# Optimization experiments

Hardware: AMD Instinct MI355X
Metric: run time of the kernel (lower is better)

## Reference

```python
import jax, jax.numpy as jnp
import numpy as np

NUM_EXPERTS = 3
INPUT_DIM = 1024
HIDDEN_DIM = 4096
OUTPUT_DIM = 1024
ROUTER_HIDDEN = 128
BATCH = 8192


def setup_inputs() -> dict:
    key = jax.random.key(0)
    ks = jax.random.split(key, 6)
    s_in = 1.0 / np.sqrt(INPUT_DIM)
    s_h = 1.0 / np.sqrt(HIDDEN_DIM)
    s_rh = 1.0 / np.sqrt(ROUTER_HIDDEN)
    return {
        "x": jax.random.normal(ks[0], (BATCH, INPUT_DIM), jnp.float32),
        "router_w1": jax.random.normal(ks[1], (INPUT_DIM, ROUTER_HIDDEN), jnp.float32) * s_in,
        "router_b1": jnp.zeros((ROUTER_HIDDEN,), jnp.float32),
        "router_w2": jax.random.normal(ks[2], (ROUTER_HIDDEN, NUM_EXPERTS), jnp.float32) * s_rh,
        "router_b2": jnp.zeros((NUM_EXPERTS,), jnp.float32),
        "expert_w1": jax.random.normal(ks[3], (NUM_EXPERTS, INPUT_DIM, HIDDEN_DIM), jnp.float32) * s_in,
        "expert_b1": jnp.zeros((NUM_EXPERTS, HIDDEN_DIM), jnp.float32),
        "expert_w2": jax.random.normal(ks[4], (NUM_EXPERTS, HIDDEN_DIM, OUTPUT_DIM), jnp.float32) * s_h,
        "expert_b2": jnp.zeros((NUM_EXPERTS, OUTPUT_DIM), jnp.float32),
    }


def reference(x, router_w1, router_b1, router_w2, router_b2,
              expert_w1, expert_b1, expert_w2, expert_b2):
    # Router: MLP -> softmax probs, hard top-1 selection (argmax)
    rh = jax.nn.relu(x @ router_w1 + router_b1)          # [B, 128]
    logits = rh @ router_w2 + router_b2                   # [B, E]
    probs = jax.nn.softmax(logits, axis=-1)
    selected = jnp.argmax(probs, axis=-1)                 # [B] int

    # Per-expert forward on all tokens (dense equivalent of masked dispatch)
    h = jax.nn.relu(jnp.einsum('bi,eih->ebh', x, expert_w1) + expert_b1[:, None, :])  # [E,B,H]
    y = jnp.einsum('ebh,eho->ebo', h, expert_w2) + expert_b2[:, None, :]              # [E,B,O]

    # Scatter-combine: each token takes its selected expert's output
    outputs = jnp.take_along_axis(
        y, selected[None, :, None], axis=0)[0]            # [B, O]

    # routing_stats: tokens per expert
    routing_stats = jnp.bincount(selected, length=NUM_EXPERTS)
    return outputs, routing_stats
```

## Files before the change

### kernel.cpp

```cpp
#include <hip/hip_runtime.h>
#include <hip/hip_bf16.h>

typedef short bf16x8 __attribute__((ext_vector_type(8)));
typedef float f32x4 __attribute__((ext_vector_type(4)));
typedef __attribute__((address_space(1))) const void gconst_t;
typedef __attribute__((address_space(3))) void lds_t;

#define DEVI __device__ __forceinline__

constexpr int BATCH   = 8192;
constexpr int IN_DIM  = 1024;
constexpr int HID     = 4096;
constexpr int OUT_DIM = 1024;
constexpr int NE      = 3;

constexpr size_t XBF_OFF  = 0;
constexpr size_t W1T_OFF  = 16777216;
constexpr size_t W2T_OFF  = W1T_OFF + 25165824;
constexpr size_t H_OFF    = W2T_OFF + 25165824;
constexpr size_t META_OFF = H_OFF + 67108864;

DEVI unsigned short f2bf(float f) {
  __hip_bfloat16 h = __float2bfloat16(f);
  return *reinterpret_cast<unsigned short*>(&h);
}

__global__ __launch_bounds__(256) void prep_kernel(
    const float* __restrict__ x, const float* __restrict__ ew1, const float* __restrict__ ew2,
    const float* __restrict__ rw1, const float* __restrict__ rb1,
    const float* __restrict__ rw2, const float* __restrict__ rb2,
    unsigned short* __restrict__ xb, unsigned short* __restrict__ w1t,
    unsigned short* __restrict__ w2t, int* __restrict__ counts, int* __restrict__ toklist) {
  __shared__ float smem[8 * 1024 + 8 * 128];
  const int b = blockIdx.x;
  const int tid = threadIdx.x;

  if (b < 1024) {
    const int t0 = b * 8;
    float* xs = smem;
    float* rh = smem + 8 * 1024;
    {
      const float4* src = (const float4*)(x + (size_t)t0 * 1024);
      float4* dstv = (float4*)xs;
      for (int i = tid; i < 2048; i += 256) dstv[i] = src[i];
    }
    __syncthreads();
    const int g = tid >> 7, hcol = tid & 127;
    float acc[4] = {0.f, 0.f, 0.f, 0.f};
    for (int k = 0; k < 1024; k += 4) {
      const float w0 = rw1[(k + 0) * 128 + hcol];
      const float w1v = rw1[(k + 1) * 128 + hcol];
      const float w2v = rw1[(k + 2) * 128 + hcol];
      const float w3v = rw1[(k + 3) * 128 + hcol];
#pragma unroll
      for (int tt = 0; tt < 4; tt++) {
        const float4 xv = *(const float4*)&xs[(g * 4 + tt) * 1024 + k];
        acc[tt] = fmaf(xv.x, w0, acc[tt]);
        acc[tt] = fmaf(xv.y, w1v, acc[tt]);
        acc[tt] = fmaf(xv.z, w2v, acc[tt]);
        acc[tt] = fmaf(xv.w, w3v, acc[tt]);
      }
    }
    const float bb1 = rb1[hcol];
#pragma unroll
    for (int tt = 0; tt < 4; tt++)
      rh[(g * 4 + tt) * 128 + hcol] = fmaxf(acc[tt] + bb1, 0.f);
    __syncthreads();
    float* lg = smem;
    if (tid < 24) {
      const int t = tid / 3, e = tid % 3;
      float s = rb2[e];
      for (int j = 0; j < 128; j++) s = fmaf(rh[t * 128 + j], rw2[j * 3 + e], s);
      lg[t * 3 + e] = s;
    }
    __syncthreads();
    if (tid < 8) {
      const float l0 = lg[tid * 3], l1 = lg[tid * 3 + 1], l2 = lg[tid * 3 + 2];
      int sel = 0; float m = l0;
      if (l1 > m) { m = l1; sel = 1; }
      if (l2 > m) { m = l2; sel = 2; }
      const int slot = atomicAdd(&counts[sel], 1);
      toklist[sel * BATCH + slot] = t0 + tid;
    }
  } else if (b < 7168) {
    float (*tile)[65] = (float(*)[65])smem;
    const float* src; unsigned short* dst; int R, C, r0, c0;
    if (b < 4096) {
      const int bb = b - 1024, e = bb / 1024, w = bb % 1024;
      src = ew1 + (size_t)e * 1024 * 4096; dst = w1t + (size_t)e * 4096 * 1024;
      R = 1024; C = 4096; r0 = (w & 15) * 64; c0 = (w >> 4) * 64;
    } else {
      const int bb = b - 4096, e = bb / 1024, w = bb % 1024;
      src = ew2 + (size_t)e * 4096 * 1024; dst = w2t + (size_t)e * 1024 * 4096;
      R = 4096; C = 1024; r0 = (w & 63) * 64; c0 = (w >> 6) * 64;
    }
    const int tr = tid >> 4;
    const int tc = (tid & 15) << 2;
#pragma unroll
    for (int i = 0; i < 4; i++) {
      const int r = tr + i * 16;
      const float4 v = *(const float4*)(src + (size_t)(r0 + r) * C + (c0 + tc));
      tile[r][tc + 0] = v.x; tile[r][tc + 1] = v.y; tile[r][tc + 2] = v.z; tile[r][tc + 3] = v.w;
    }
    __syncthreads();
#pragma unroll
    for (int i = 0; i < 4; i++) {
      const int c = tr + i * 16;
      ushort4 o;
      o.x = f2bf(tile[tc + 0][c]);
      o.y = f2bf(tile[tc + 1][c]);
      o.z = f2bf(tile[tc + 2][c]);
      o.w = f2bf(tile[tc + 3][c]);
      *(ushort4*)(dst + (size_t)(c0 + c) * R + (r0 + tc)) = o;
    }
  } else {
    const float4* xv4 = (const float4*)x;
    const int total = BATCH * IN_DIM / 4;
    for (int i = (b - 7168) * 256 + tid; i < total; i += 512 * 256) {
      const float4 v = xv4[i];
      ushort4 o;
      o.x = f2bf(v.x); o.y = f2bf(v.y); o.z = f2bf(v.z); o.w = f2bf(v.w);
      ((ushort4*)xb)[i] = o;
    }
  }
}

template <int MODE>
__global__ __launch_bounds__(256, 2) void moe_gemm(
    const unsigned short* __restrict__ Abase, const unsigned short* __restrict__ Ball,
    const float* __restrict__ biasAll, unsigned short* __restrict__ Hout,
    float* __restrict__ Yout, const int* __restrict__ toklist, const int* __restrict__ counts,
    float* __restrict__ tail) {
  constexpr int N = (MODE == 0) ? HID : OUT_DIM;
  constexpr int K = (MODE == 0) ? IN_DIM : HID;
  constexpr int NT = K / 64;

  if (MODE == 0 && blockIdx.x == 0 && blockIdx.y == 0 && threadIdx.x < NE)
    tail[threadIdx.x] = (float)counts[threadIdx.x];

  const int c0 = counts[0], c1 = counts[1], c2 = counts[2];
  const int mb0 = (c0 + 127) >> 7, mb1 = (c1 + 127) >> 7, mb2 = (c2 + 127) >> 7;
  const int bx = blockIdx.x;
  int e, mblk;
  if (bx < mb0) { e = 0; mblk = bx; }
  else if (bx < mb0 + mb1) { e = 1; mblk = bx - mb0; }
  else if (bx < mb0 + mb1 + mb2) { e = 2; mblk = bx - mb0 - mb1; }
  else return;
  const int cnt = (e == 0) ? c0 : (e == 1) ? c1 : c2;
  const int m0 = mblk * 128;
  const int n0 = blockIdx.y * 128;
  const int off_e = (e > 0 ? c0 : 0) + (e > 1 ? c1 : 0);
  const unsigned short* Bmat = Ball + (size_t)e * ((size_t)N * K);
  const float* bias = biasAll + (size_t)e * N;

  __shared__ unsigned short Ab[2][128 * 64];
  __shared__ unsigned short Bb[2][128 * 64];

  const int tid = threadIdx.x;
  const unsigned short* aptr[4];
  const unsigned short* bptr[4];
  unsigned ldsoff[4];
#pragma unroll
  for (int l = 0; l < 4; l++) {
    const unsigned o = l * 4096u + (unsigned)tid * 16u;
    const unsigned p = o ^ (((o >> 7) & 7u) << 4);
    const int row = (int)(p >> 7);
    const int kel = (int)((p & 127u) >> 1);
    ldsoff[l] = o;
    bptr[l] = Bmat + (size_t)(n0 + row) * K + kel;
    int slot = m0 + row; if (slot > cnt - 1) slot = cnt - 1;
    const size_t arow = (MODE == 0) ? (size_t)toklist[e * BATCH + slot]
                                    : (size_t)(off_e + slot);
    aptr[l] = Abase + arow * K + kel;
  }

  f32x4 acc[4][4];
#pragma unroll
  for (int i = 0; i < 4; i++)
#pragma unroll
    for (int j = 0; j < 4; j++) acc[i][j] = {0.f, 0.f, 0.f, 0.f};

  const int lane = tid & 63;
  const int wave = tid >> 6;
  const int wm = (wave >> 1) * 64;
  const int wn = (wave & 1) * 64;
  const int fr = lane & 15;
  const int fc = lane >> 4;
  const unsigned sx = (unsigned)((fr & 7) << 4);

  auto STAGE = [&](int buf, int kofs) {
#pragma unroll
    for (int l = 0; l < 4; l++)
      __builtin_amdgcn_global_load_lds((gconst_t*)(aptr[l] + kofs),
                                       (lds_t*)((char*)&Ab[buf][0] + ldsoff[l]), 16, 0, 0);
#pragma unroll
    for (int l = 0; l < 4; l++)
      __builtin_amdgcn_global_load_lds((gconst_t*)(bptr[l] + kofs),
                                       (lds_t*)((char*)&Bb[buf][0] + ldsoff[l]), 16, 0, 0);
  };

  STAGE(0, 0);
  asm volatile("s_waitcnt vmcnt(0)" ::: "memory");
  __builtin_amdgcn_s_barrier();

  for (int t = 0; t < NT; ++t) {
    const int cur = t & 1;
    bf16x8 af[2][4], bv[2][4];
#pragma unroll
    for (int ks = 0; ks < 2; ks++) {
#pragma unroll
      for (int m = 0; m < 4; m++) {
        const unsigned row = (unsigned)(wm + m * 16 + fr);
        const unsigned addr = ((row << 7) + (unsigned)(ks * 64 + fc * 16)) ^ sx;
        af[ks][m] = *(const bf16x8*)((const char*)&Ab[cur][0] + addr);
      }
#pragma unroll
      for (int n = 0; n < 4; n++) {
        const unsigned row = (unsigned)(wn + n * 16 + fr);
        const unsigned addr = ((row << 7) + (unsigned)(ks * 64 + fc * 16)) ^ sx;
        bv[ks][n] = *(const bf16x8*)((const char*)&Bb[cur][0] + addr);
      }
    }
    asm volatile("s_waitcnt lgkmcnt(0)" ::: "memory");
    __builtin_amdgcn_sched_barrier(0);
    __builtin_amdgcn_s_barrier();
    if (t + 1 < NT) STAGE(cur ^ 1, (t + 1) * 64);
#pragma unroll
    for (int ks = 0; ks < 2; ks++)
#pragma unroll
      for (int m = 0; m < 4; m++)
#pragma unroll
        for (int n = 0; n < 4; n++)
          acc[m][n] = __builtin_amdgcn_mfma_f32_16x16x32_bf16(af[ks][m], bv[ks][n], acc[m][n], 0, 0, 0);
    if (t + 1 < NT) {
      asm volatile("s_waitcnt vmcnt(0)" ::: "memory");
      __builtin_amdgcn_s_barrier();
    }
  }

  const int crow = (lane >> 4) * 4;
  const int ccol = lane & 15;
#pragma unroll
  for (int mi = 0; mi < 4; mi++) {
#pragma unroll
    for (int r = 0; r < 4; r++) {
      const int slot = m0 + wm + mi * 16 + crow + r;
      if (slot >= cnt) continue;
      if (MODE == 0) {
        unsigned short* hrow = Hout + (size_t)(off_e + slot) * HID;
#pragma unroll
        for (int ni = 0; ni < 4; ni++) {
          const int n = n0 + wn + ni * 16 + ccol;
          const float v = acc[mi][ni][r] + bias[n];
          hrow[n] = f2bf(fmaxf(v, 0.f));
        }
      } else {
        const int tok = toklist[e * BATCH + slot];
        float* yrow = Yout + (size_t)tok * OUT_DIM;
#pragma unroll
        for (int ni = 0; ni < 4; ni++) {
          const int n = n0 + wn + ni * 16 + ccol;
          yrow[n] = acc[mi][ni][r] + bias[n];
        }
      }
    }
  }
}

extern "C" void kernel_launch(void* const* d_in, const int* in_sizes, int n_in,
                              void* d_out, int out_size, void* d_ws, size_t ws_size,
                              hipStream_t stream) {
  const float* x   = (const float*)d_in[0];
  const float* rw1 = (const float*)d_in[1];
  const float* rb1 = (const float*)d_in[2];
  const float* rw2 = (const float*)d_in[3];
  const float* rb2 = (const float*)d_in[4];
  const float* ew1 = (const float*)d_in[5];
  const float* eb1 = (const float*)d_in[6];
  const float* ew2 = (const float*)d_in[7];
  const float* eb2 = (const float*)d_in[8];
  float* out = (float*)d_out;

  char* ws = (char*)d_ws;
  unsigned short* xb  = (unsigned short*)(ws + XBF_OFF);
  unsigned short* w1t = (unsigned short*)(ws + W1T_OFF);
  unsigned short* w2t = (unsigned short*)(ws + W2T_OFF);
  unsigned short* h   = (unsigned short*)(ws + H_OFF);
  int* counts  = (int*)(ws + META_OFF);
  int* toklist = counts + 16;
  float* tail = out + (size_t)BATCH * OUT_DIM;

  hipMemsetAsync(counts, 0, 64, stream);
  prep_kernel<<<7680, 256, 0, stream>>>(x, ew1, ew2, rw1, rb1, rw2, rb2,
                                        xb, w1t, w2t, counts, toklist);
  moe_gemm<0><<<dim3(66, 32), 256, 0, stream>>>(xb, w1t, eb1, h, nullptr, toklist, counts, tail);
  moe_gemm<1><<<dim3(66, 8), 256, 0, stream>>>(h, w2t, eb2, nullptr, out, toklist, counts, tail);
}
```

Baseline: 368.3 us.

## Enlarge GEMM tiles to 256-row blocks with 512 threads and K=32 steps

Reworks the expert GEMM kernels to use 512-thread blocks with 256-row M tiles (256x256 for the first GEMM, 256x128 for the second), a 32-wide K step with a 4-way XOR swizzle, and the next-stage prefetch issued before the LDS reads. MFMA sections are wrapped in setprio. The router path in the prep kernel now reads x directly from global memory instead of staging it in a large LDS buffer, which shrinks shared memory. The aim is more data reuse per tile and higher occupancy in prep, at the cost of more accumulator registers and more padding waste for partial expert tiles.

```diff
diff --git a/kernel.cpp b/kernel.cpp
--- a/kernel.cpp
+++ b/kernel.cpp
@@ -31,21 +31,15 @@
     const float* __restrict__ rw2, const float* __restrict__ rb2,
     unsigned short* __restrict__ xb, unsigned short* __restrict__ w1t,
     unsigned short* __restrict__ w2t, int* __restrict__ counts, int* __restrict__ toklist) {
-  __shared__ float smem[8 * 1024 + 8 * 128];
+  __shared__ float psm[64 * 65];
   const int b = blockIdx.x;
   const int tid = threadIdx.x;
 
   if (b < 1024) {
     const int t0 = b * 8;
-    float* xs = smem;
-    float* rh = smem + 8 * 1024;
-    {
-      const float4* src = (const float4*)(x + (size_t)t0 * 1024);
-      float4* dstv = (float4*)xs;
-      for (int i = tid; i < 2048; i += 256) dstv[i] = src[i];
-    }
-    __syncthreads();
-    const int g = tid >> 7, hcol = tid & 127;
+    const int hcol = tid & 127;
+    const int g = tid >> 7;
+    const float* xrow0 = x + (size_t)(t0 + g * 4) * 1024;
     float acc[4] = {0.f, 0.f, 0.f, 0.f};
     for (int k = 0; k < 1024; k += 4) {
       const float w0 = rw1[(k + 0) * 128 + hcol];
@@ -54,7 +48,7 @@
       const float w3v = rw1[(k + 3) * 128 + hcol];
 #pragma unroll
       for (int tt = 0; tt < 4; tt++) {
-        const float4 xv = *(const float4*)&xs[(g * 4 + tt) * 1024 + k];
+        const float4 xv = *(const float4*)(xrow0 + (size_t)tt * 1024 + k);
         acc[tt] = fmaf(xv.x, w0, acc[tt]);
         acc[tt] = fmaf(xv.y, w1v, acc[tt]);
         acc[tt] = fmaf(xv.z, w2v, acc[tt]);
@@ -64,13 +58,13 @@
     const float bb1 = rb1[hcol];
 #pragma unroll
     for (int tt = 0; tt < 4; tt++)
-      rh[(g * 4 + tt) * 128 + hcol] = fmaxf(acc[tt] + bb1, 0.f);
-    __syncthreads();
-    float* lg = smem;
+      psm[(g * 4 + tt) * 128 + hcol] = fmaxf(acc[tt] + bb1, 0.f);
+    __syncthreads();
+    float* lg = psm + 1024;
     if (tid < 24) {
       const int t = tid / 3, e = tid % 3;
       float s = rb2[e];
-      for (int j = 0; j < 128; j++) s = fmaf(rh[t * 128 + j], rw2[j * 3 + e], s);
+      for (int j = 0; j < 128; j++) s = fmaf(psm[t * 128 + j], rw2[j * 3 + e], s);
       lg[t * 3 + e] = s;
     }
     __syncthreads();
@@ -83,7 +77,7 @@
       toklist[sel * BATCH + slot] = t0 + tid;
     }
   } else if (b < 7168) {
-    float (*tile)[65] = (float(*)[65])smem;
+    float (*tile)[65] = (float(*)[65])psm;
     const float* src; unsigned short* dst; int R, C, r0, c0;
     if (b < 4096) {
       const int bb = b - 1024, e = bb / 1024, w = bb % 1024;
@@ -126,20 +120,24 @@
 }
 
 template <int MODE>
-__global__ __launch_bounds__(256, 2) void moe_gemm(
+__global__ __launch_bounds__(512, 2) void moe_gemm(
     const unsigned short* __restrict__ Abase, const unsigned short* __restrict__ Ball,
     const float* __restrict__ biasAll, unsigned short* __restrict__ Hout,
     float* __restrict__ Yout, const int* __restrict__ toklist, const int* __restrict__ counts,
     float* __restrict__ tail) {
-  constexpr int N = (MODE == 0) ? HID : OUT_DIM;
-  constexpr int K = (MODE == 0) ? IN_DIM : HID;
-  constexpr int NT = K / 64;
-
-  if (MODE == 0 && blockIdx.x == 0 && blockIdx.y == 0 && threadIdx.x < NE)
-    tail[threadIdx.x] = (float)counts[threadIdx.x];
+  constexpr int BN = (MODE == 0) ? 256 : 128;
+  constexpr int N  = (MODE == 0) ? HID : OUT_DIM;
+  constexpr int K  = (MODE == 0) ? IN_DIM : HID;
+  constexpr int NT = K / 32;
+  constexpr int NF = BN / 64;
+  constexpr int BLOADS = BN / 128;
+
+  const int tid = threadIdx.x;
+  if (MODE == 0 && blockIdx.x == 0 && blockIdx.y == 0 && tid < NE)
+    tail[tid] = (float)counts[tid];
 
   const int c0 = counts[0], c1 = counts[1], c2 = counts[2];
-  const int mb0 = (c0 + 127) >> 7, mb1 = (c1 + 127) >> 7, mb2 = (c2 + 127) >> 7;
+  const int mb0 = (c0 + 255) >> 8, mb1 = (c1 + 255) >> 8, mb2 = (c2 + 255) >> 8;
   const int bx = blockIdx.x;
   int e, mblk;
   if (bx < mb0) { e = 0; mblk = bx; }
@@ -147,101 +145,98 @@
   else if (bx < mb0 + mb1 + mb2) { e = 2; mblk = bx - mb0 - mb1; }
   else return;
   const int cnt = (e == 0) ? c0 : (e == 1) ? c1 : c2;
-  const int m0 = mblk * 128;
-  const int n0 = blockIdx.y * 128;
+  const int m0 = mblk * 256;
+  const int n0 = blockIdx.y * BN;
   const int off_e = (e > 0 ? c0 : 0) + (e > 1 ? c1 : 0);
   const unsigned short* Bmat = Ball + (size_t)e * ((size_t)N * K);
   const float* bias = biasAll + (size_t)e * N;
 
-  __shared__ unsigned short Ab[2][128 * 64];
-  __shared__ unsigned short Bb[2][128 * 64];
-
-  const int tid = threadIdx.x;
-  const unsigned short* aptr[4];
-  const unsigned short* bptr[4];
-  unsigned ldsoff[4];
-#pragma unroll
-  for (int l = 0; l < 4; l++) {
-    const unsigned o = l * 4096u + (unsigned)tid * 16u;
-    const unsigned p = o ^ (((o >> 7) & 7u) << 4);
-    const int row = (int)(p >> 7);
-    const int kel = (int)((p & 127u) >> 1);
-    ldsoff[l] = o;
-    bptr[l] = Bmat + (size_t)(n0 + row) * K + kel;
+  __shared__ unsigned short Ab[2][256 * 32];
+  __shared__ unsigned short Bb[2][BN * 32];
+
+  const unsigned short* asrc[2];
+  unsigned aoff[2];
+  const unsigned short* bsrc[BLOADS];
+  unsigned boff[BLOADS];
+#pragma unroll
+  for (int l = 0; l < 2; l++) {
+    const unsigned o = l * 8192u + (unsigned)tid * 16u;
+    const unsigned p = o ^ (((o >> 6) & 3u) << 4);
+    const int row = (int)(o >> 6);
+    const int kel = (int)((p & 63u) >> 1);
+    aoff[l] = o;
     int slot = m0 + row; if (slot > cnt - 1) slot = cnt - 1;
     const size_t arow = (MODE == 0) ? (size_t)toklist[e * BATCH + slot]
                                     : (size_t)(off_e + slot);
-    aptr[l] = Abase + arow * K + kel;
-  }
-
-  f32x4 acc[4][4];
-#pragma unroll
-  for (int i = 0; i < 4; i++)
-#pragma unroll
-    for (int j = 0; j < 4; j++) acc[i][j] = {0.f, 0.f, 0.f, 0.f};
+    asrc[l] = Abase + arow * K + kel;
+  }
+#pragma unroll
+  for (int l = 0; l < BLOADS; l++) {
+    const unsigned o = l * 8192u + (unsigned)tid * 16u;
+    const unsigned p = o ^ (((o >> 6) & 3u) << 4);
+    const int row = (int)(o >> 6);
+    const int kel = (int)((p & 63u) >> 1);
+    boff[l] = o;
+    bsrc[l] = Bmat + (size_t)(n0 + row) * K + kel;
+  }
+
+  f32x4 acc[8][NF];
+#pragma unroll
+  for (int i = 0; i < 8; i++)
+#pragma unroll
+    for (int j = 0; j < NF; j++) acc[i][j] = {0.f, 0.f, 0.f, 0.f};
 
   const int lane = tid & 63;
   const int wave = tid >> 6;
-  const int wm = (wave >> 1) * 64;
-  const int wn = (wave & 1) * 64;
+  const int wm = (wave >> 2) * 128;
+  const int wn = (wave & 3) * (BN / 4);
   const int fr = lane & 15;
   const int fc = lane >> 4;
-  const unsigned sx = (unsigned)((fr & 7) << 4);
 
   auto STAGE = [&](int buf, int kofs) {
 #pragma unroll
-    for (int l = 0; l < 4; l++)
-      __builtin_amdgcn_global_load_lds((gconst_t*)(aptr[l] + kofs),
-                                       (lds_t*)((char*)&Ab[buf][0] + ldsoff[l]), 16, 0, 0);
-#pragma unroll
-    for (int l = 0; l < 4; l++)
-      __builtin_amdgcn_global_load_lds((gconst_t*)(bptr[l] + kofs),
-                                       (lds_t*)((char*)&Bb[buf][0] + ldsoff[l]), 16, 0, 0);
+    for (int l = 0; l < 2; l++)
+      __builtin_amdgcn_global_load_lds((gconst_t*)(asrc[l] + kofs),
+                                       (lds_t*)((char*)&Ab[buf][0] + aoff[l]), 16, 0, 0);
+#pragma unroll
+    for (int l = 0; l < BLOADS; l++)
+      __builtin_amdgcn_global_load_lds((gconst_t*)(bsrc[l] + kofs),
+                                       (lds_t*)((char*)&Bb[buf][0] + boff[l]), 16, 0, 0);
   };
 
   STAGE(0, 0);
-  asm volatile("s_waitcnt vmcnt(0)" ::: "memory");
-  __builtin_amdgcn_s_barrier();
+  __syncthreads();
 
   for (int t = 0; t < NT; ++t) {
     const int cur = t & 1;
-    bf16x8 af[2][4], bv[2][4];
-#pragma unroll
-    for (int ks = 0; ks < 2; ks++) {
-#pragma unroll
-      for (int m = 0; m < 4; m++) {
-        const unsigned row = (unsigned)(wm + m * 16 + fr);
-        const unsigned addr = ((row << 7) + (unsigned)(ks * 64 + fc * 16)) ^ sx;
-        af[ks][m] = *(const bf16x8*)((const char*)&Ab[cur][0] + addr);
-      }
-#pragma unroll
-      for (int n = 0; n < 4; n++) {
-        const unsigned row = (unsigned)(wn + n * 16 + fr);
-        const unsigned addr = ((row << 7) + (unsigned)(ks * 64 + fc * 16)) ^ sx;
-        bv[ks][n] = *(const bf16x8*)((const char*)&Bb[cur][0] + addr);
-      }
-    }
-    asm volatile("s_waitcnt lgkmcnt(0)" ::: "memory");
-    __builtin_amdgcn_sched_barrier(0);
-    __builtin_amdgcn_s_barrier();
-    if (t + 1 < NT) STAGE(cur ^ 1, (t + 1) * 64);
-#pragma unroll
-    for (int ks = 0; ks < 2; ks++)
-#pragma unroll
-      for (int m = 0; m < 4; m++)
-#pragma unroll
-        for (int n = 0; n < 4; n++)
-          acc[m][n] = __builtin_amdgcn_mfma_f32_16x16x32_bf16(af[ks][m], bv[ks][n], acc[m][n], 0, 0, 0);
-    if (t + 1 < NT) {
-      asm volatile("s_waitcnt vmcnt(0)" ::: "memory");
-      __builtin_amdgcn_s_barrier();
-    }
+    if (t + 1 < NT) STAGE(cur ^ 1, (t + 1) * 32);
+    bf16x8 af[8], bv[NF];
+#pragma unroll
+    for (int m = 0; m < 8; m++) {
+      const unsigned row = (unsigned)(wm + m * 16 + fr);
+      const unsigned addr = ((row << 6) + (unsigned)(fc << 4)) ^ ((row & 3u) << 4);
+      af[m] = *(const bf16x8*)((const char*)&Ab[cur][0] + addr);
+    }
+#pragma unroll
+    for (int n = 0; n < NF; n++) {
+      const unsigned row = (unsigned)(wn + n * 16 + fr);
+      const unsigned addr = ((row << 6) + (unsigned)(fc << 4)) ^ ((row & 3u) << 4);
+      bv[n] = *(const bf16x8*)((const char*)&Bb[cur][0] + addr);
+    }
+    __builtin_amdgcn_s_setprio(1);
+#pragma unroll
+    for (int m = 0; m < 8; m++)
+#pragma unroll
+      for (int n = 0; n < NF; n++)
+        acc[m][n] = __builtin_amdgcn_mfma_f32_16x16x32_bf16(af[m], bv[n], acc[m][n], 0, 0, 0);
+    __builtin_amdgcn_s_setprio(0);
+    __syncthreads();
   }
 
   const int crow = (lane >> 4) * 4;
   const int ccol = lane & 15;
 #pragma unroll
-  for (int mi = 0; mi < 4; mi++) {
+  for (int mi = 0; mi < 8; mi++) {
 #pragma unroll
     for (int r = 0; r < 4; r++) {
       const int slot = m0 + wm + mi * 16 + crow + r;
@@ -249,7 +244,7 @@
       if (MODE == 0) {
         unsigned short* hrow = Hout + (size_t)(off_e + slot) * HID;
 #pragma unroll
-        for (int ni = 0; ni < 4; ni++) {
+        for (int ni = 0; ni < NF; ni++) {
           const int n = n0 + wn + ni * 16 + ccol;
           const float v = acc[mi][ni][r] + bias[n];
           hrow[n] = f2bf(fmaxf(v, 0.f));
@@ -258,7 +253,7 @@
         const int tok = toklist[e * BATCH + slot];
         float* yrow = Yout + (size_t)tok * OUT_DIM;
 #pragma unroll
-        for (int ni = 0; ni < 4; ni++) {
+        for (int ni = 0; ni < NF; ni++) {
           const int n = n0 + wn + ni * 16 + ccol;
           yrow[n] = acc[mi][ni][r] + bias[n];
         }
@@ -293,6 +288,6 @@
   hipMemsetAsync(counts, 0, 64, stream);
   prep_kernel<<<7680, 256, 0, stream>>>(x, ew1, ew2, rw1, rb1, rw2, rb2,
                                         xb, w1t, w2t, counts, toklist);
-  moe_gemm<0><<<dim3(66, 32), 256, 0, stream>>>(xb, w1t, eb1, h, nullptr, toklist, counts, tail);
-  moe_gemm<1><<<dim3(66, 8), 256, 0, stream>>>(h, w2t, eb2, nullptr, out, toklist, counts, tail);
-}
+  moe_gemm<0><<<dim3(34, 16), 512, 0, stream>>>(xb, w1t, eb1, h, nullptr, toklist, counts, tail);
+  moe_gemm<1><<<dim3(34, 8), 512, 0, stream>>>(h, w2t, eb2, nullptr, out, toklist, counts, tail);
+}
```

New measurement: 473.3 us. 1.29x slower.
